# Performance work log

Hardware: AMD Instinct MI355X
Metric: run time of the kernel (lower is better)

## Reference

```python
import jax, jax.numpy as jnp
import numpy as np

N_CLASSES = 1000  # init kwarg n_classes
BIG = 1e24        # diagonal fill used by get_center_distances


def setup_inputs() -> dict:
    key = jax.random.key(0)
    k1, k2 = jax.random.split(key)
    embeddings = jax.random.normal(k1, (400000, 64), dtype=jnp.float32)
    target = jax.random.randint(k2, (400000,), 0, N_CLASSES)
    return {"embeddings": embeddings, "target": target}


def reference(embeddings, target):
    # Training-mode IILoss forward (returned loss does not depend on running buffers).
    n = embeddings.shape[0]
    ones = jnp.ones((n,), embeddings.dtype)
    counts = jax.ops.segment_sum(ones, target, num_segments=N_CLASSES)          # [C]
    sums = jax.ops.segment_sum(embeddings, target, num_segments=N_CLASSES)      # [C, D]
    mu = sums / jnp.maximum(counts, 1.0)[:, None]                                # per-class mean

    # intra_spread = sum_i ||e_i - mu[target_i]||^2 / n  (single fused pass)
    diff = embeddings - mu[target]
    intra_spread = jnp.sum(diff * diff) / n

    # pairwise squared distances between centers of classes present in the batch
    sq = jnp.sum(mu * mu, axis=1)                                                # [C]
    dists = sq[:, None] + sq[None, :] - 2.0 * (mu @ mu.T)                        # [C, C]
    present = counts > 0
    mask = present[:, None] & present[None, :] & ~jnp.eye(N_CLASSES, dtype=bool)
    dists = jnp.where(mask, dists, jnp.asarray(BIG, dists.dtype))
    inter_separation = -jnp.min(dists)
    return (intra_spread, inter_separation)
```

## Files before the change

kernel.cpp:

```cpp
#include <hip/hip_runtime.h>

#define NCLS 1000
#define DIM 64
#define CURW 32
#define SPLIT 8
#define STAGE 512
#define CAP 1024
#define TPB 256
#define TILE 32
#define NTA 32
#define NPAIR (NTA * (NTA + 1) / 2)

struct Ws {
    unsigned minkey;
    unsigned pad_[31];
    int      cur[NCLS * CURW];
    float    mu[NCLS * DIM];
    float    sq[NCLS];
    float    part[NCLS * SPLIT * DIM];
    float    part_ssq[NCLS * SPLIT];
    float    cls_ssq[NCLS];
    float    cls_mt[NCLS];
};

struct RedSm  { int sidx[STAGE]; float facc[4][DIM]; float fssq[4]; };
struct PairSm { float As[TILE][DIM + 1]; float Bs[TILE][DIM + 1];
                float sqa[TILE], sqb[TILE]; int pa[TILE], pb[TILE];
                unsigned redm[4]; };
struct FinSm  { double sd[TPB], md[TPB]; };

__device__ __forceinline__ unsigned fkey(float x) {
    unsigned b = __float_as_uint(x);
    return (b & 0x80000000u) ? ~b : (b | 0x80000000u);
}
__device__ __forceinline__ float funkey(unsigned k) {
    return (k & 0x80000000u) ? __uint_as_float(k & 0x7FFFFFFFu)
                             : __uint_as_float(~k);
}

__global__ __launch_bounds__(TPB) void f_zero(Ws* ws) {
    const int gtid = blockIdx.x * TPB + threadIdx.x;
    for (int i = gtid; i < NCLS * CURW; i += (int)gridDim.x * TPB) ws->cur[i] = 0;
    if (gtid == 0) ws->minkey = fkey(1.0e24f);
}

__global__ __launch_bounds__(TPB) void f_scatter(const int* __restrict__ tgt, int n,
                                                 Ws* ws, int* __restrict__ bucket) {
    for (int r = blockIdx.x * TPB + threadIdx.x; r < n; r += (int)gridDim.x * TPB) {
        const int c = tgt[r];
        const int p = atomicAdd(&ws->cur[c * CURW], 1);
        if (p < CAP) bucket[c * CAP + p] = r;
    }
}

__global__ __launch_bounds__(TPB) void f_reduce(const float* __restrict__ emb,
                                                const int* __restrict__ bucket,
                                                Ws* __restrict__ ws) {
    __shared__ RedSm sm;
    const int vb   = blockIdx.x;
    const int c    = vb / SPLIT;
    const int sp   = vb % SPLIT;
    const int t    = threadIdx.x;
    const int lane = t & 63;
    const int w    = t >> 6;
    const int cnt  = min(ws->cur[c * CURW], CAP);
    const int i0   = (cnt * sp) / SPLIT;
    const int i1   = (cnt * (sp + 1)) / SPLIT;
    const int base = c * CAP + i0;
    const int m    = i1 - i0;

    float acc = 0.f, ssq = 0.f;
    for (int s0 = 0; s0 < m; s0 += STAGE) {
        const int mm = min(STAGE, m - s0);
        __syncthreads();
        for (int i = t; i < mm; i += TPB) sm.sidx[i] = bucket[base + s0 + i];
        __syncthreads();
        int p = w;
        for (; p + 28 < mm; p += 32) {
            const int r0 = sm.sidx[p];      const int r1 = sm.sidx[p + 4];
            const int r2 = sm.sidx[p + 8];  const int r3 = sm.sidx[p + 12];
            const int r4 = sm.sidx[p + 16]; const int r5 = sm.sidx[p + 20];
            const int r6 = sm.sidx[p + 24]; const int r7 = sm.sidx[p + 28];
            const float v0 = emb[(size_t)r0 * DIM + lane];
            const float v1 = emb[(size_t)r1 * DIM + lane];
            const float v2 = emb[(size_t)r2 * DIM + lane];
            const float v3 = emb[(size_t)r3 * DIM + lane];
            const float v4 = emb[(size_t)r4 * DIM + lane];
            const float v5 = emb[(size_t)r5 * DIM + lane];
            const float v6 = emb[(size_t)r6 * DIM + lane];
            const float v7 = emb[(size_t)r7 * DIM + lane];
            acc += v0 + v1 + v2 + v3 + v4 + v5 + v6 + v7;
            ssq += v0 * v0 + v1 * v1 + v2 * v2 + v3 * v3
                 + v4 * v4 + v5 * v5 + v6 * v6 + v7 * v7;
        }
        for (; p < mm; p += 4) {
            const float v0 = emb[(size_t)sm.sidx[p] * DIM + lane];
            acc += v0;
            ssq += v0 * v0;
        }
    }
    __syncthreads();
    sm.facc[w][lane] = acc;
    float s = ssq;
    for (int o = 32; o; o >>= 1) s += __shfl_down(s, o);
    if (lane == 0) sm.fssq[w] = s;
    __syncthreads();
    if (t < DIM)
        ws->part[vb * DIM + t] = sm.facc[0][t] + sm.facc[1][t]
                               + sm.facc[2][t] + sm.facc[3][t];
    if (t == 0)
        ws->part_ssq[vb] = sm.fssq[0] + sm.fssq[1] + sm.fssq[2] + sm.fssq[3];
}

__global__ __launch_bounds__(TPB) void f_centers(Ws* ws) {
    const int c    = blockIdx.x * 4 + (threadIdx.x >> 6);
    const int lane = threadIdx.x & 63;
    if (c >= NCLS) return;
    const int cnt = min(ws->cur[c * CURW], CAP);
    float v = 0.f;
    #pragma unroll
    for (int s2 = 0; s2 < SPLIT; ++s2) v += ws->part[(c * SPLIT + s2) * DIM + lane];
    const float m = v / (float)max(cnt, 1);
    ws->mu[c * DIM + lane] = m;
    float p = m * m;
    for (int o = 32; o; o >>= 1) p += __shfl_down(p, o);
    if (lane == 0) {
        ws->sq[c]     = p;
        ws->cls_mt[c] = cnt ? (float)cnt * p : 0.f;
        float q = 0.f;
        #pragma unroll
        for (int s2 = 0; s2 < SPLIT; ++s2) q += ws->part_ssq[c * SPLIT + s2];
        ws->cls_ssq[c] = q;
    }
}

__global__ __launch_bounds__(TPB) void f_pairs(Ws* ws) {
    __shared__ PairSm sm;
    const int t = threadIdx.x;
    int rem = blockIdx.x, ta = 0;
    while (rem >= NTA - ta) { rem -= NTA - ta; ++ta; }
    const int tb = ta + rem;

    for (int i = t; i < TILE * (DIM / 4); i += TPB) {
        const int r = i >> 4, c4 = (i & 15) * 4;
        const int ga = ta * TILE + r;
        const int gb = tb * TILE + r;
        float4 va = make_float4(0.f, 0.f, 0.f, 0.f);
        float4 vb = make_float4(0.f, 0.f, 0.f, 0.f);
        if (ga < NCLS) va = *reinterpret_cast<const float4*>(&ws->mu[ga * DIM + c4]);
        if (gb < NCLS) vb = *reinterpret_cast<const float4*>(&ws->mu[gb * DIM + c4]);
        sm.As[r][c4 + 0] = va.x; sm.As[r][c4 + 1] = va.y;
        sm.As[r][c4 + 2] = va.z; sm.As[r][c4 + 3] = va.w;
        sm.Bs[r][c4 + 0] = vb.x; sm.Bs[r][c4 + 1] = vb.y;
        sm.Bs[r][c4 + 2] = vb.z; sm.Bs[r][c4 + 3] = vb.w;
    }
    if (t < TILE) {
        const int ga = ta * TILE + t;
        sm.pa[t]  = (ga < NCLS) ? (min(ws->cur[ga * CURW], CAP) > 0) : 0;
        sm.sqa[t] = (ga < NCLS) ? ws->sq[ga] : 0.f;
    } else if (t < 2 * TILE) {
        const int tt = t - TILE;
        const int gb = tb * TILE + tt;
        sm.pb[tt]  = (gb < NCLS) ? (min(ws->cur[gb * CURW], CAP) > 0) : 0;
        sm.sqb[tt] = (gb < NCLS) ? ws->sq[gb] : 0.f;
    }
    __syncthreads();

    const int ty2 = (t >> 4) * 2;
    const int tx2 = (t & 15) * 2;
    float dot[2][2] = {{0.f, 0.f}, {0.f, 0.f}};
    #pragma unroll 8
    for (int k = 0; k < DIM; ++k) {
        float av[2], bv[2];
        av[0] = sm.As[ty2][k];     av[1] = sm.As[ty2 + 1][k];
        bv[0] = sm.Bs[tx2][k];     bv[1] = sm.Bs[tx2 + 1][k];
        dot[0][0] += av[0] * bv[0]; dot[0][1] += av[0] * bv[1];
        dot[1][0] += av[1] * bv[0]; dot[1][1] += av[1] * bv[1];
    }

    float best = 3.0e38f;
    #pragma unroll
    for (int i = 0; i < 2; ++i) {
        #pragma unroll
        for (int j = 0; j < 2; ++j) {
            const int ga = ta * TILE + ty2 + i;
            const int gb = tb * TILE + tx2 + j;
            const bool valid = sm.pa[ty2 + i] && sm.pb[tx2 + j] && (ga != gb);
            const float dd = sm.sqa[ty2 + i] + sm.sqb[tx2 + j] - 2.f * dot[i][j];
            if (valid) best = fminf(best, dd);
        }
    }
    for (int o = 32; o; o >>= 1) best = fminf(best, __shfl_down(best, o));
    if ((t & 63) == 0) sm.redm[t >> 6] = fkey(best);
    __syncthreads();
    if (t == 0) {
        unsigned mk = sm.redm[0];
        #pragma unroll
        for (int q = 1; q < 4; ++q) mk = min(mk, sm.redm[q]);
        atomicMin(&ws->minkey, mk);
    }
}

__global__ __launch_bounds__(TPB) void f_final(const Ws* ws, float* out, int n) {
    __shared__ FinSm sm;
    const int t = threadIdx.x;
    double a = 0.0, b = 0.0;
    for (int i = t; i < NCLS; i += TPB) { a += (double)ws->cls_ssq[i]; b += (double)ws->cls_mt[i]; }
    sm.sd[t] = a; sm.md[t] = b;
    __syncthreads();
    for (int s = 128; s >= 1; s >>= 1) {
        if (t < s) { sm.sd[t] += sm.sd[t + s]; sm.md[t] += sm.md[t + s]; }
        __syncthreads();
    }
    if (t == 0) {
        out[0] = (float)((sm.sd[0] - sm.md[0]) / (double)n);
        out[1] = -funkey(ws->minkey);
    }
}

extern "C" void kernel_launch(void* const* d_in, const int* in_sizes, int n_in,
                              void* d_out, int out_size, void* d_ws, size_t ws_size,
                              hipStream_t stream) {
    const float* emb = (const float*)d_in[0];
    const int*   tgt = (const int*)d_in[1];
    float* out = (float*)d_out;
    const int n = in_sizes[1];
    Ws* ws = (Ws*)d_ws;
    int* bucket = (int*)((char*)d_ws + sizeof(Ws));

    f_zero   <<<125, TPB, 0, stream>>>(ws);
    f_scatter<<<1024, TPB, 0, stream>>>(tgt, n, ws, bucket);
    f_reduce <<<NCLS * SPLIT, TPB, 0, stream>>>(emb, bucket, ws);
    f_centers<<<NCLS / 4, TPB, 0, stream>>>(ws);
    f_pairs  <<<NPAIR, TPB, 0, stream>>>(ws);
    f_final  <<<1, TPB, 0, stream>>>(ws, out, n);
}
```

Baseline: 67.10 us.

## Vectorize class reduction with float4 loads, halve split, fuse final into pairs

The per-class reduction now loads embedding rows as float4, with 16 threads per row, and combines the 16 row-groups through a shared-memory tree. The split per class drops from 8 to 4 blocks. The separate final kernel is removed: the last pairs block, found with an atomic counter, performs the final sums and writes the output. This saves one launch and lowers load instruction count, at the cost of fewer reduce blocks and a serial tail in the last block.

After: 71.77 us. 1.07x slower.

```diff
diff --git a/kernel.cpp b/kernel.cpp
--- a/kernel.cpp
+++ b/kernel.cpp
@@ -3,7 +3,7 @@
 #define NCLS 1000
 #define DIM 64
 #define CURW 32
-#define SPLIT 8
+#define SPLIT 4
 #define STAGE 512
 #define CAP 1024
 #define TPB 256
@@ -13,7 +13,8 @@
 
 struct Ws {
     unsigned minkey;
-    unsigned pad_[31];
+    int      fincnt;
+    unsigned pad_[30];
     int      cur[NCLS * CURW];
     float    mu[NCLS * DIM];
     float    sq[NCLS];
@@ -23,11 +24,11 @@
     float    cls_mt[NCLS];
 };
 
-struct RedSm  { int sidx[STAGE]; float facc[4][DIM]; float fssq[4]; };
+struct RedSm  { int sidx[STAGE]; float lds[16][DIM + 4]; float ssq_red[4]; };
 struct PairSm { float As[TILE][DIM + 1]; float Bs[TILE][DIM + 1];
                 float sqa[TILE], sqb[TILE]; int pa[TILE], pb[TILE];
-                unsigned redm[4]; };
-struct FinSm  { double sd[TPB], md[TPB]; };
+                unsigned redm[4]; int isLast;
+                double sd[TPB], md[TPB]; };
 
 __device__ __forceinline__ unsigned fkey(float x) {
     unsigned b = __float_as_uint(x);
@@ -41,7 +42,7 @@
 __global__ __launch_bounds__(TPB) void f_zero(Ws* ws) {
     const int gtid = blockIdx.x * TPB + threadIdx.x;
     for (int i = gtid; i < NCLS * CURW; i += (int)gridDim.x * TPB) ws->cur[i] = 0;
-    if (gtid == 0) ws->minkey = fkey(1.0e24f);
+    if (gtid == 0) { ws->minkey = fkey(1.0e24f); ws->fincnt = 0; }
 }
 
 __global__ __launch_bounds__(TPB) void f_scatter(const int* __restrict__ tgt, int n,
@@ -58,58 +59,66 @@
                                                 Ws* __restrict__ ws) {
     __shared__ RedSm sm;
     const int vb   = blockIdx.x;
-    const int c    = vb / SPLIT;
-    const int sp   = vb % SPLIT;
+    const int c    = vb >> 2;
+    const int sp   = vb & (SPLIT - 1);
     const int t    = threadIdx.x;
-    const int lane = t & 63;
-    const int w    = t >> 6;
+    const int slot = t & 15;
+    const int g    = t >> 4;
     const int cnt  = min(ws->cur[c * CURW], CAP);
     const int i0   = (cnt * sp) / SPLIT;
     const int i1   = (cnt * (sp + 1)) / SPLIT;
     const int base = c * CAP + i0;
     const int m    = i1 - i0;
 
-    float acc = 0.f, ssq = 0.f;
+    float ax = 0.f, ay = 0.f, az = 0.f, aw = 0.f, ssq = 0.f;
     for (int s0 = 0; s0 < m; s0 += STAGE) {
         const int mm = min(STAGE, m - s0);
         __syncthreads();
         for (int i = t; i < mm; i += TPB) sm.sidx[i] = bucket[base + s0 + i];
         __syncthreads();
-        int p = w;
-        for (; p + 28 < mm; p += 32) {
-            const int r0 = sm.sidx[p];      const int r1 = sm.sidx[p + 4];
-            const int r2 = sm.sidx[p + 8];  const int r3 = sm.sidx[p + 12];
-            const int r4 = sm.sidx[p + 16]; const int r5 = sm.sidx[p + 20];
-            const int r6 = sm.sidx[p + 24]; const int r7 = sm.sidx[p + 28];
-            const float v0 = emb[(size_t)r0 * DIM + lane];
-            const float v1 = emb[(size_t)r1 * DIM + lane];
-            const float v2 = emb[(size_t)r2 * DIM + lane];
-            const float v3 = emb[(size_t)r3 * DIM + lane];
-            const float v4 = emb[(size_t)r4 * DIM + lane];
-            const float v5 = emb[(size_t)r5 * DIM + lane];
-            const float v6 = emb[(size_t)r6 * DIM + lane];
-            const float v7 = emb[(size_t)r7 * DIM + lane];
-            acc += v0 + v1 + v2 + v3 + v4 + v5 + v6 + v7;
-            ssq += v0 * v0 + v1 * v1 + v2 * v2 + v3 * v3
-                 + v4 * v4 + v5 * v5 + v6 * v6 + v7 * v7;
-        }
-        for (; p < mm; p += 4) {
-            const float v0 = emb[(size_t)sm.sidx[p] * DIM + lane];
-            acc += v0;
-            ssq += v0 * v0;
-        }
-    }
-    __syncthreads();
-    sm.facc[w][lane] = acc;
+        int i = g;
+        for (; i + 48 < mm; i += 64) {
+            const int r0 = sm.sidx[i];      const int r1 = sm.sidx[i + 16];
+            const int r2 = sm.sidx[i + 32]; const int r3 = sm.sidx[i + 48];
+            const float4 v0 = *reinterpret_cast<const float4*>(emb + (size_t)r0 * DIM + slot * 4);
+            const float4 v1 = *reinterpret_cast<const float4*>(emb + (size_t)r1 * DIM + slot * 4);
+            const float4 v2 = *reinterpret_cast<const float4*>(emb + (size_t)r2 * DIM + slot * 4);
+            const float4 v3 = *reinterpret_cast<const float4*>(emb + (size_t)r3 * DIM + slot * 4);
+            ax += v0.x + v1.x + v2.x + v3.x;
+            ay += v0.y + v1.y + v2.y + v3.y;
+            az += v0.z + v1.z + v2.z + v3.z;
+            aw += v0.w + v1.w + v2.w + v3.w;
+            ssq += v0.x * v0.x + v0.y * v0.y + v0.z * v0.z + v0.w * v0.w
+                 + v1.x * v1.x + v1.y * v1.y + v1.z * v1.z + v1.w * v1.w
+                 + v2.x * v2.x + v2.y * v2.y + v2.z * v2.z + v2.w * v2.w
+                 + v3.x * v3.x + v3.y * v3.y + v3.z * v3.z + v3.w * v3.w;
+        }
+        for (; i < mm; i += 16) {
+            const int r0 = sm.sidx[i];
+            const float4 v0 = *reinterpret_cast<const float4*>(emb + (size_t)r0 * DIM + slot * 4);
+            ax += v0.x; ay += v0.y; az += v0.z; aw += v0.w;
+            ssq += v0.x * v0.x + v0.y * v0.y + v0.z * v0.z + v0.w * v0.w;
+        }
+    }
+    __syncthreads();
+    sm.lds[g][slot * 4 + 0] = ax; sm.lds[g][slot * 4 + 1] = ay;
+    sm.lds[g][slot * 4 + 2] = az; sm.lds[g][slot * 4 + 3] = aw;
+    __syncthreads();
+    for (int s = 8; s >= 1; s >>= 1) {
+        if (g < s) {
+            #pragma unroll
+            for (int k = 0; k < 4; ++k)
+                sm.lds[g][slot * 4 + k] += sm.lds[g + s][slot * 4 + k];
+        }
+        __syncthreads();
+    }
     float s = ssq;
     for (int o = 32; o; o >>= 1) s += __shfl_down(s, o);
-    if (lane == 0) sm.fssq[w] = s;
-    __syncthreads();
-    if (t < DIM)
-        ws->part[vb * DIM + t] = sm.facc[0][t] + sm.facc[1][t]
-                               + sm.facc[2][t] + sm.facc[3][t];
+    if ((t & 63) == 0) sm.ssq_red[t >> 6] = s;
+    __syncthreads();
+    if (t < DIM) ws->part[vb * DIM + t] = sm.lds[0][t];
     if (t == 0)
-        ws->part_ssq[vb] = sm.fssq[0] + sm.fssq[1] + sm.fssq[2] + sm.fssq[3];
+        ws->part_ssq[vb] = sm.ssq_red[0] + sm.ssq_red[1] + sm.ssq_red[2] + sm.ssq_red[3];
 }
 
 __global__ __launch_bounds__(TPB) void f_centers(Ws* ws) {
@@ -134,7 +143,7 @@
     }
 }
 
-__global__ __launch_bounds__(TPB) void f_pairs(Ws* ws) {
+__global__ __launch_bounds__(TPB) void f_pairs(Ws* ws, float* out, int n) {
     __shared__ PairSm sm;
     const int t = threadIdx.x;
     int rem = blockIdx.x, ta = 0;
@@ -198,23 +207,28 @@
         #pragma unroll
         for (int q = 1; q < 4; ++q) mk = min(mk, sm.redm[q]);
         atomicMin(&ws->minkey, mk);
-    }
-}
-
-__global__ __launch_bounds__(TPB) void f_final(const Ws* ws, float* out, int n) {
-    __shared__ FinSm sm;
-    const int t = threadIdx.x;
-    double a = 0.0, b = 0.0;
-    for (int i = t; i < NCLS; i += TPB) { a += (double)ws->cls_ssq[i]; b += (double)ws->cls_mt[i]; }
-    sm.sd[t] = a; sm.md[t] = b;
-    __syncthreads();
-    for (int s = 128; s >= 1; s >>= 1) {
-        if (t < s) { sm.sd[t] += sm.sd[t + s]; sm.md[t] += sm.md[t + s]; }
-        __syncthreads();
-    }
-    if (t == 0) {
-        out[0] = (float)((sm.sd[0] - sm.md[0]) / (double)n);
-        out[1] = -funkey(ws->minkey);
+        __threadfence();
+        sm.isLast = (atomicAdd(&ws->fincnt, 1) == NPAIR - 1);
+    }
+    __syncthreads();
+
+    if (sm.isLast) {
+        double a = 0.0, b = 0.0;
+        for (int i = t; i < NCLS; i += TPB) {
+            a += (double)ws->cls_ssq[i];
+            b += (double)ws->cls_mt[i];
+        }
+        sm.sd[t] = a; sm.md[t] = b;
+        __syncthreads();
+        for (int s = 128; s >= 1; s >>= 1) {
+            if (t < s) { sm.sd[t] += sm.sd[t + s]; sm.md[t] += sm.md[t + s]; }
+            __syncthreads();
+        }
+        if (t == 0) {
+            const unsigned mk = atomicOr(&ws->minkey, 0u);
+            out[0] = (float)((sm.sd[0] - sm.md[0]) / (double)n);
+            out[1] = -funkey(mk);
+        }
     }
 }
 
@@ -232,6 +246,5 @@
     f_scatter<<<1024, TPB, 0, stream>>>(tgt, n, ws, bucket);
     f_reduce <<<NCLS * SPLIT, TPB, 0, stream>>>(emb, bucket, ws);
     f_centers<<<NCLS / 4, TPB, 0, stream>>>(ws);
-    f_pairs  <<<NPAIR, TPB, 0, stream>>>(ws);
-    f_final  <<<1, TPB, 0, stream>>>(ws, out, n);
-}
+    f_pairs  <<<NPAIR, TPB, 0, stream>>>(ws, out, n);
+}
```
